# Performance work log

Measured on AMD Instinct MI355X. Metric: run time of the kernel, lower is better.

Reference implementation:

```python
import jax, jax.numpy as jnp
import numpy as np

B, F, V, D, K = 16384, 39, 30000, 16, 20
EPS = 1e-5


def bn_eval(x, g, b):
    # inference-mode BatchNorm1d with running_mean=0, running_var=1
    return g * x / jnp.sqrt(1.0 + EPS) + b


def setup_inputs() -> dict:
    key = jax.random.key(0)
    ks = jax.random.split(key, 12)
    x = jax.random.randint(ks[0], (B, F), 0, V)
    emb_table = jax.random.normal(ks[1], (F * V, D), dtype=jnp.float32) * 0.05
    w_c = jax.random.normal(ks[2], (F, F * D), dtype=jnp.float32) * 0.05
    w0 = jax.random.normal(ks[3], (1024, F * D), dtype=jnp.float32) * 0.04
    w1 = jax.random.normal(ks[4], (512, 1024), dtype=jnp.float32) * 0.03
    w_out = jax.random.normal(ks[5], (1, 512), dtype=jnp.float32) * 0.04
    return {
        'x': x, 'emb_table': emb_table,
        'w_c': w_c, 'b_c': jnp.zeros((F,)), 'g_c': jnp.ones((F,)), 'be_c': jnp.zeros((F,)),
        'w0': w0, 'b0': jnp.zeros((1024,)), 'g0': jnp.ones((1024,)), 'be0': jnp.zeros((1024,)),
        'w1': w1, 'b1': jnp.zeros((512,)), 'g1': jnp.ones((512,)), 'be1': jnp.zeros((512,)),
        'w_out': w_out, 'b_out': jnp.zeros((1,)),
    }


def reference(x, emb_table, w_c, b_c, g_c, be_c, w0, b0, g0, be0,
              w1, b1, g1, be1, w_out, b_out):
    offsets = jnp.arange(F, dtype=x.dtype) * V          # per-field offsets
    idx = x + offsets[None, :]                          # [B, F]
    emb = emb_table[idx]                                # [B, F, D] gather

    # controller_mlp: flatten (batch, D, F) layout like torch transpose(1,2)
    flat = jnp.transpose(emb, (0, 2, 1)).reshape(B, F * D)
    h = jax.nn.relu(bn_eval(flat @ w_c.T + b_c, g_c, be_c))
    scores = jax.nn.softmax(h, axis=1)                  # [B, F]

    # kmax_pooling: top-k field indices, sorted ascending, gather weights
    _, kidx = jax.lax.top_k(scores, K)
    kidx = jnp.sort(kidx, axis=1)                       # [B, K]
    w = jnp.take_along_axis(scores, kidx, axis=1)       # [B, K]

    # forward_select: gather selected field embeddings, weight them
    sel = jnp.take_along_axis(emb, kidx[:, :, None], axis=1)  # [B, K, D]
    weighted = sel * w[:, :, None]

    # scatter back into full field slots (unselected fields are zero)
    full = jnp.zeros((B, F, D), weighted.dtype)
    bidx = jnp.arange(B)[:, None]
    full = full.at[bidx, kidx].set(weighted)            # [B, F, D]

    z = jnp.transpose(full, (0, 2, 1)).reshape(B, F * D)
    z = jax.nn.relu(bn_eval(z @ w0.T + b0, g0, be0))
    z = jax.nn.relu(bn_eval(z @ w1.T + b1, g1, be1))
    out = jax.nn.sigmoid(z @ w_out.T + b_out)           # [B, 1]
    return out.squeeze(-1)
```

## Files before the change

### kernel.cpp

```cpp
#include <hip/hip_runtime.h>
#include <math.h>

#define B_SZ 16384
#define F_N 39
#define V_N 30000
#define D_N 16
#define K_SEL 20
#define FD 624
#define KP0 640
#define NCP 48
#define N0 1024
#define N1 512
#define CBR 16
#define ALD 648

typedef unsigned short u16;
typedef __attribute__((ext_vector_type(8))) short bf16x8;
typedef __attribute__((ext_vector_type(8))) unsigned short u16x8;
typedef __attribute__((ext_vector_type(4))) float f32x4;
typedef __attribute__((ext_vector_type(4))) unsigned short u16x4;

__device__ __forceinline__ u16 f2bf(float v) {
    union { float f; unsigned u; } x; x.f = v;
    unsigned r = x.u + 0x7fff + ((x.u >> 16) & 1);
    return (u16)(r >> 16);
}
__device__ __forceinline__ float bf2f(u16 v) {
    union { unsigned u; float f; } x; x.u = ((unsigned)v) << 16;
    return x.f;
}

#define GLD16(gp, lp) __builtin_amdgcn_global_load_lds( \
    (const __attribute__((address_space(1))) unsigned int*)(gp), \
    (__attribute__((address_space(3))) unsigned int*)(lp), 16, 0, 0)

#define PREP_W0 (N0 * KP0)
#define PREP_W1 (N1 * N0)
#define PREP_WC (NCP * KP0)
#define PREP_TOT (PREP_W0 + PREP_W1 + PREP_WC + 3 * NCP)

__global__ __launch_bounds__(256) void prep_all_kernel(
    const float* __restrict__ w0, const float* __restrict__ w1,
    const float* __restrict__ w_c, const float* __restrict__ b_c,
    const float* __restrict__ g_c, const float* __restrict__ be_c,
    u16* __restrict__ w0b, u16* __restrict__ w1b, u16* __restrict__ wcb,
    float* __restrict__ bcp, float* __restrict__ gcp, float* __restrict__ becp)
{
    int i = blockIdx.x * blockDim.x + threadIdx.x;
    if (i < PREP_W0) {
        int n = i / KP0, kk = i - n * KP0;
        float v = 0.f;
        if (kk < FD) v = w0[n * FD + (kk & 15) * F_N + (kk >> 4)];
        w0b[i] = f2bf(v);
        return;
    }
    i -= PREP_W0;
    if (i < PREP_W1) { w1b[i] = f2bf(w1[i]); return; }
    i -= PREP_W1;
    if (i < PREP_WC) {
        int n = i / KP0, kk = i - n * KP0;
        float v = 0.f;
        if (n < F_N && kk < FD) v = w_c[n * FD + (kk & 15) * F_N + (kk >> 4)];
        wcb[i] = f2bf(v);
        return;
    }
    i -= PREP_WC;
    if (i < 3 * NCP) {
        int which = i / NCP, n = i - which * NCP;
        float v = 0.f;
        if (n < F_N) v = (which == 0) ? b_c[n] : (which == 1) ? g_c[n] : be_c[n];
        ((which == 0) ? bcp : (which == 1) ? gcp : becp)[n] = v;
    }
}

__global__ __launch_bounds__(256) void fused_controller_kernel(
    const int* __restrict__ x, const float* __restrict__ emb_table,
    const u16* __restrict__ wcb, const float* __restrict__ bcp,
    const float* __restrict__ gcp, const float* __restrict__ becp,
    u16* __restrict__ zb)
{
    __shared__ __align__(16) u16 Al[CBR * ALD];
    __shared__ float vv[CBR][49];
    __shared__ f32x4 part[4][64][3];
    __shared__ float selw[CBR][F_N];

    const int t    = threadIdx.x;
    const int wave = t >> 6;
    const int lane = t & 63;
    const int b0   = blockIdx.x * CBR;

    for (int p = t; p < CBR * F_N; p += 256) {
        const int row = p / F_N;
        const int f   = p - row * F_N;
        const int xi  = x[b0 * F_N + p];
        const float4* src = (const float4*)(emb_table + (size_t)(xi + f * V_N) * D_N);
        float4 v0 = src[0], v1 = src[1], v2 = src[2], v3 = src[3];
        u16x8 o0 = { f2bf(v0.x), f2bf(v0.y), f2bf(v0.z), f2bf(v0.w),
                     f2bf(v1.x), f2bf(v1.y), f2bf(v1.z), f2bf(v1.w) };
        u16x8 o1 = { f2bf(v2.x), f2bf(v2.y), f2bf(v2.z), f2bf(v2.w),
                     f2bf(v3.x), f2bf(v3.y), f2bf(v3.z), f2bf(v3.w) };
        *(u16x8*)&Al[row * ALD + f * D_N]     = o0;
        *(u16x8*)&Al[row * ALD + f * D_N + 8] = o1;
    }
    __syncthreads();

    const int m = lane & 15;
    const int q = lane >> 4;
    f32x4 acc0 = {}, acc1 = {}, acc2 = {};
    {
        const u16* ap  = &Al[m * ALD + wave * 160 + q * 8];
        const u16* bp0 = wcb + (size_t)(0  + m) * KP0 + wave * 160 + q * 8;
        const u16* bp1 = wcb + (size_t)(16 + m) * KP0 + wave * 160 + q * 8;
        const u16* bp2 = wcb + (size_t)(32 + m) * KP0 + wave * 160 + q * 8;
        #pragma unroll
        for (int k = 0; k < 5; ++k) {
            bf16x8 af = *(const bf16x8*)ap;
            bf16x8 b0 = *(const bf16x8*)bp0;
            bf16x8 b1 = *(const bf16x8*)bp1;
            bf16x8 b2 = *(const bf16x8*)bp2;
            acc0 = __builtin_amdgcn_mfma_f32_16x16x32_bf16(af, b0, acc0, 0, 0, 0);
            acc1 = __builtin_amdgcn_mfma_f32_16x16x32_bf16(af, b1, acc1, 0, 0, 0);
            acc2 = __builtin_amdgcn_mfma_f32_16x16x32_bf16(af, b2, acc2, 0, 0, 0);
            ap += 32; bp0 += 32; bp1 += 32; bp2 += 32;
        }
    }
    part[wave][lane][0] = acc0;
    part[wave][lane][1] = acc1;
    part[wave][lane][2] = acc2;
    __syncthreads();

    {
        f32x4 r0 = part[0][lane][0] + part[1][lane][0] + part[2][lane][0] + part[3][lane][0];
        f32x4 r1 = part[0][lane][1] + part[1][lane][1] + part[2][lane][1] + part[3][lane][1];
        f32x4 r2 = part[0][lane][2] + part[1][lane][2] + part[2][lane][2] + part[3][lane][2];

        const float rs = rsqrtf(1.0f + 1e-5f);
        if (q == wave) {
            #pragma unroll
            for (int j = 0; j < 3; ++j) {
                const f32x4 a = (j == 0) ? r0 : (j == 1) ? r1 : r2;
                const int n = j * 16 + m;
                const float gn = gcp[n] * rs;
                const float bn = becp[n];
                const float bi = bcp[n];
                #pragma unroll
                for (int r = 0; r < 4; ++r)
                    vv[wave * 4 + r][n] = fmaxf(fmaf(gn, a[r] + bi, bn), 0.f);
            }
        }
    }
    __syncthreads();

    {
        const int row = wave * 4 + (lane >> 4);
        const int fl  = lane & 15;
        float e[3] = {0.f, 0.f, 0.f};
        float mloc = -1e30f;
        #pragma unroll
        for (int it = 0; it < 3; ++it) {
            const int f = fl + 16 * it;
            if (f < F_N) { e[it] = vv[row][f]; mloc = fmaxf(mloc, e[it]); }
        }
        mloc = fmaxf(mloc, __shfl_xor(mloc, 1, 64));
        mloc = fmaxf(mloc, __shfl_xor(mloc, 2, 64));
        mloc = fmaxf(mloc, __shfl_xor(mloc, 4, 64));
        mloc = fmaxf(mloc, __shfl_xor(mloc, 8, 64));
        float sloc = 0.f;
        #pragma unroll
        for (int it = 0; it < 3; ++it) {
            const int f = fl + 16 * it;
            if (f < F_N) { e[it] = expf(e[it] - mloc); sloc += e[it]; }
        }
        sloc += __shfl_xor(sloc, 1, 64);
        sloc += __shfl_xor(sloc, 2, 64);
        sloc += __shfl_xor(sloc, 4, 64);
        sloc += __shfl_xor(sloc, 8, 64);
        const float inv = 1.f / sloc;
        #pragma unroll
        for (int it = 0; it < 3; ++it) {
            const int f = fl + 16 * it;
            if (f < F_N) vv[row][f] = e[it];
        }

        int rank[3] = {};
        for (int gg = 0; gg < F_N; ++gg) {
            const float o = vv[row][gg];
            #pragma unroll
            for (int it = 0; it < 3; ++it) {
                const int f = fl + 16 * it;
                if (f < F_N)
                    rank[it] += (o > e[it] || (o == e[it] && gg < f)) ? 1 : 0;
            }
        }
        #pragma unroll
        for (int it = 0; it < 3; ++it) {
            const int f = fl + 16 * it;
            if (f < F_N)
                selw[row][f] = (rank[it] < K_SEL) ? e[it] * inv : 0.f;
        }
    }
    __syncthreads();

    for (int gp = t; gp < CBR * 40; gp += 256) {
        const int row  = gp & 15;
        const int slot = gp >> 4;
        u16* dst = zb + (size_t)(b0 + row) * KP0 + slot * D_N;
        u16x8 o0 = {0,0,0,0,0,0,0,0}, o1 = {0,0,0,0,0,0,0,0};
        if (slot < F_N) {
            const float w = selw[row][slot];
            u16x8 a0 = *(u16x8*)&Al[row * ALD + slot * D_N];
            u16x8 a1 = *(u16x8*)&Al[row * ALD + slot * D_N + 8];
            #pragma unroll
            for (int k = 0; k < 8; ++k) {
                o0[k] = f2bf(bf2f(a0[k]) * w);
                o1[k] = f2bf(bf2f(a1[k]) * w);
            }
        }
        *(u16x8*)dst = o0;
        *(u16x8*)(dst + 8) = o1;
    }
}

template<int MODE>
__global__ __launch_bounds__(256) void gemm_mfma_bn_relu(
    const u16* __restrict__ A, const u16* __restrict__ W,
    const float* __restrict__ bias, const float* __restrict__ g,
    const float* __restrict__ be, u16* __restrict__ Cout,
    int M, int N, int Kp,
    const float* __restrict__ w_out, float* __restrict__ outp)
{
    __shared__ __align__(16) u16 As[2][128 * 32];
    __shared__ __align__(16) u16 Bs[2][128 * 32];

    const int t    = threadIdx.x;
    const int wave = t >> 6;
    const int lane = t & 63;
    const int wm   = wave >> 1, wn = wave & 1;
    const int m0   = blockIdx.x * 128;
    const int n0   = blockIdx.y * 128;

    const int lr    = lane >> 2;
    const int swz_u = (lane & 3) ^ ((lane >> 3) & 3);
    const u16* gA0 = A + (size_t)(m0 + wave * 32 + lr) * Kp + swz_u * 8;
    const u16* gB0 = W + (size_t)(n0 + wave * 32 + lr) * Kp + swz_u * 8;
    const size_t kstep16 = 16 * (size_t)Kp;
    const int oA0 = (wave * 32) * 32;
    const int oA1 = (wave * 32 + 16) * 32;

    const int q    = lane >> 4;
    const int lr16 = lane & 15;

    int aoff[4], boff[4];
    #pragma unroll
    for (int i = 0; i < 4; ++i) {
        int ra = wm * 64 + i * 16 + lr16;
        aoff[i] = ra * 32 + ((q ^ ((ra >> 1) & 3)) * 8);
        int rb = wn * 64 + i * 16 + lr16;
        boff[i] = rb * 32 + ((q ^ ((rb >> 1) & 3)) * 8);
    }

    GLD16(gA0,           &As[0][oA0]);
    GLD16(gA0 + kstep16, &As[0][oA1]);
    GLD16(gB0,           &Bs[0][oA0]);
    GLD16(gB0 + kstep16, &Bs[0][oA1]);
    gA0 += 32; gB0 += 32;

    f32x4 acc[4][4] = {};
    int buf = 0;

    for (int k0 = 0; k0 < Kp; k0 += 32) {
        __syncthreads();
        if (k0 + 32 < Kp) {
            GLD16(gA0,           &As[buf ^ 1][oA0]);
            GLD16(gA0 + kstep16, &As[buf ^ 1][oA1]);
            GLD16(gB0,           &Bs[buf ^ 1][oA0]);
            GLD16(gB0 + kstep16, &Bs[buf ^ 1][oA1]);
            gA0 += 32; gB0 += 32;
        }

        bf16x8 af[4], bfr[4];
        #pragma unroll
        for (int i = 0; i < 4; ++i) af[i]  = *(const bf16x8*)&As[buf][aoff[i]];
        #pragma unroll
        for (int j = 0; j < 4; ++j) bfr[j] = *(const bf16x8*)&Bs[buf][boff[j]];

        #pragma unroll
        for (int i = 0; i < 4; ++i)
            #pragma unroll
            for (int j = 0; j < 4; ++j)
                acc[i][j] = __builtin_amdgcn_mfma_f32_16x16x32_bf16(
                    af[i], bfr[j], acc[i][j], 0, 0, 0);
        buf ^= 1;
    }

    const float rs = rsqrtf(1.0f + 1e-5f);
    if (MODE == 0) {
        #pragma unroll
        for (int j = 0; j < 4; ++j) {
            const int n = n0 + wn * 64 + j * 16 + lr16;
            const float bn_g = g[n] * rs;
            const float bn_b = be[n];
            const float bi   = bias[n];
            #pragma unroll
            for (int i = 0; i < 4; ++i) {
                const int mbase = m0 + wm * 64 + i * 16 + q * 4;
                #pragma unroll
                for (int r = 0; r < 4; ++r) {
                    float v = acc[i][j][r] + bi;
                    v = fmaxf(fmaf(bn_g, v, bn_b), 0.f);
                    Cout[(size_t)(mbase + r) * N + n] = f2bf(v);
                }
            }
        }
    } else {
        float s[4][4] = {};
        #pragma unroll
        for (int j = 0; j < 4; ++j) {
            const int n = n0 + wn * 64 + j * 16 + lr16;
            const float bn_g = g[n] * rs;
            const float bn_b = be[n];
            const float bi   = bias[n];
            const float wo   = w_out[n];
            #pragma unroll
            for (int i = 0; i < 4; ++i)
                #pragma unroll
                for (int r = 0; r < 4; ++r) {
                    float v = acc[i][j][r] + bi;
                    v = fmaxf(fmaf(bn_g, v, bn_b), 0.f);
                    s[i][r] = fmaf(v, wo, s[i][r]);
                }
        }
        #pragma unroll
        for (int i = 0; i < 4; ++i)
            #pragma unroll
            for (int r = 0; r < 4; ++r) {
                float v = s[i][r];
                v += __shfl_xor(v, 1, 64);
                v += __shfl_xor(v, 2, 64);
                v += __shfl_xor(v, 4, 64);
                v += __shfl_xor(v, 8, 64);
                s[i][r] = v;
            }
        if (lr16 == 0) {
            #pragma unroll
            for (int i = 0; i < 4; ++i) {
                const int mbase = m0 + wm * 64 + i * 16 + q * 4;
                #pragma unroll
                for (int r = 0; r < 4; ++r)
                    atomicAdd(&outp[mbase + r], s[i][r]);
            }
        }
    }
}

__global__ __launch_bounds__(256) void sigmoid_kernel(
    const float* __restrict__ outp, const float* __restrict__ b_out,
    float* __restrict__ out)
{
    const int b = blockIdx.x * 256 + threadIdx.x;
    out[b] = 1.f / (1.f + expf(-(outp[b] + b_out[0])));
}

extern "C" void kernel_launch(void* const* d_in, const int* in_sizes, int n_in,
                              void* d_out, int out_size, void* d_ws, size_t ws_size,
                              hipStream_t stream)
{
    const int*   x     = (const int*)  d_in[0];
    const float* emb   = (const float*)d_in[1];
    const float* w_c   = (const float*)d_in[2];
    const float* b_c   = (const float*)d_in[3];
    const float* g_c   = (const float*)d_in[4];
    const float* be_c  = (const float*)d_in[5];
    const float* w0    = (const float*)d_in[6];
    const float* b0    = (const float*)d_in[7];
    const float* g0    = (const float*)d_in[8];
    const float* be0   = (const float*)d_in[9];
    const float* w1    = (const float*)d_in[10];
    const float* b1    = (const float*)d_in[11];
    const float* g1    = (const float*)d_in[12];
    const float* be1   = (const float*)d_in[13];
    const float* w_out = (const float*)d_in[14];
    const float* b_out = (const float*)d_in[15];
    float* out = (float*)d_out;

    u16*   zb    = (u16*)d_ws;
    u16*   w0b   = zb    + (size_t)B_SZ * KP0;
    u16*   h0b   = w0b   + (size_t)N0 * KP0;
    u16*   w1b   = h0b   + (size_t)B_SZ * N0;
    u16*   wcb   = w1b   + (size_t)N1 * N0;
    float* outp  = (float*)(wcb + (size_t)NCP * KP0);
    float* bcp   = outp + B_SZ;
    float* gcp   = bcp + NCP;
    float* becp  = gcp + NCP;

    prep_all_kernel<<<(PREP_TOT + 255) / 256, 256, 0, stream>>>(
        w0, w1, w_c, b_c, g_c, be_c, w0b, w1b, wcb, bcp, gcp, becp);

    fused_controller_kernel<<<B_SZ / CBR, 256, 0, stream>>>(
        x, emb, wcb, bcp, gcp, becp, zb);

    gemm_mfma_bn_relu<0><<<dim3(B_SZ / 128, N0 / 128), 256, 0, stream>>>(
        zb, w0b, b0, g0, be0, h0b, B_SZ, N0, KP0, nullptr, nullptr);

    hipMemsetAsync(outp, 0, B_SZ * sizeof(float), stream);

    gemm_mfma_bn_relu<1><<<dim3(B_SZ / 128, N1 / 128), 256, 0, stream>>>(
        h0b, w1b, b1, g1, be1, nullptr, B_SZ, N1, N0, w_out, outp);

    sigmoid_kernel<<<B_SZ / 256, 256, 0, stream>>>(outp, b_out, out);
}
```

Measured before the change: 223.3 us.

## Enlarge GEMM0 tile to 256x128, fold outp zeroing into prep, unroll gather

The first MLP GEMM moves to its own kernel with 256x128 block tiles, where each wave computes 64x128 outputs through a 4x8 MFMA accumulator grid. This raises operand reuse per LDS load and halves the number of blocks along M. The hipMemsetAsync on the output accumulator is removed and the zeroing is done inside the prep kernel instead. The embedding gather loop is manually unrolled so all index loads are issued up front. The larger tile needs more registers and LDS, which may lower occupancy.

```diff
diff --git a/kernel.cpp b/kernel.cpp
--- a/kernel.cpp
+++ b/kernel.cpp
@@ -37,14 +37,15 @@
 #define PREP_W0 (N0 * KP0)
 #define PREP_W1 (N1 * N0)
 #define PREP_WC (NCP * KP0)
-#define PREP_TOT (PREP_W0 + PREP_W1 + PREP_WC + 3 * NCP)
+#define PREP_TOT (PREP_W0 + PREP_W1 + PREP_WC + 3 * NCP + B_SZ)
 
 __global__ __launch_bounds__(256) void prep_all_kernel(
     const float* __restrict__ w0, const float* __restrict__ w1,
     const float* __restrict__ w_c, const float* __restrict__ b_c,
     const float* __restrict__ g_c, const float* __restrict__ be_c,
     u16* __restrict__ w0b, u16* __restrict__ w1b, u16* __restrict__ wcb,
-    float* __restrict__ bcp, float* __restrict__ gcp, float* __restrict__ becp)
+    float* __restrict__ bcp, float* __restrict__ gcp, float* __restrict__ becp,
+    float* __restrict__ outp)
 {
     int i = blockIdx.x * blockDim.x + threadIdx.x;
     if (i < PREP_W0) {
@@ -70,7 +71,10 @@
         float v = 0.f;
         if (n < F_N) v = (which == 0) ? b_c[n] : (which == 1) ? g_c[n] : be_c[n];
         ((which == 0) ? bcp : (which == 1) ? gcp : becp)[n] = v;
-    }
+        return;
+    }
+    i -= 3 * NCP;
+    if (i < B_SZ) outp[i] = 0.f;
 }
 
 __global__ __launch_bounds__(256) void fused_controller_kernel(
@@ -89,18 +93,30 @@
     const int lane = t & 63;
     const int b0   = blockIdx.x * CBR;
 
-    for (int p = t; p < CBR * F_N; p += 256) {
-        const int row = p / F_N;
-        const int f   = p - row * F_N;
-        const int xi  = x[b0 * F_N + p];
-        const float4* src = (const float4*)(emb_table + (size_t)(xi + f * V_N) * D_N);
-        float4 v0 = src[0], v1 = src[1], v2 = src[2], v3 = src[3];
-        u16x8 o0 = { f2bf(v0.x), f2bf(v0.y), f2bf(v0.z), f2bf(v0.w),
-                     f2bf(v1.x), f2bf(v1.y), f2bf(v1.z), f2bf(v1.w) };
-        u16x8 o1 = { f2bf(v2.x), f2bf(v2.y), f2bf(v2.z), f2bf(v2.w),
-                     f2bf(v3.x), f2bf(v3.y), f2bf(v3.z), f2bf(v3.w) };
-        *(u16x8*)&Al[row * ALD + f * D_N]     = o0;
-        *(u16x8*)&Al[row * ALD + f * D_N + 8] = o1;
+    {
+        const int p0 = t, p1 = t + 256, p2 = t + 512;
+        const int xi0 = x[b0 * F_N + p0];
+        const int xi1 = x[b0 * F_N + p1];
+        const int xi2 = (p2 < CBR * F_N) ? x[b0 * F_N + p2] : 0;
+        const int pp[3] = { p0, p1, p2 };
+        const int xx[3] = { xi0, xi1, xi2 };
+        #pragma unroll
+        for (int s = 0; s < 3; ++s) {
+            const int p = pp[s];
+            if (p < CBR * F_N) {
+                const int row = p / F_N;
+                const int f   = p - row * F_N;
+                const float4* src =
+                    (const float4*)(emb_table + (size_t)(xx[s] + f * V_N) * D_N);
+                float4 v0 = src[0], v1 = src[1], v2 = src[2], v3 = src[3];
+                u16x8 o0 = { f2bf(v0.x), f2bf(v0.y), f2bf(v0.z), f2bf(v0.w),
+                             f2bf(v1.x), f2bf(v1.y), f2bf(v1.z), f2bf(v1.w) };
+                u16x8 o1 = { f2bf(v2.x), f2bf(v2.y), f2bf(v2.z), f2bf(v2.w),
+                             f2bf(v3.x), f2bf(v3.y), f2bf(v3.z), f2bf(v3.w) };
+                *(u16x8*)&Al[row * ALD + f * D_N]     = o0;
+                *(u16x8*)&Al[row * ALD + f * D_N + 8] = o1;
+            }
+        }
     }
     __syncthreads();
 
@@ -221,12 +237,103 @@
     }
 }
 
-template<int MODE>
-__global__ __launch_bounds__(256) void gemm_mfma_bn_relu(
+__global__ __launch_bounds__(256) void gemm0_256_kernel(
     const u16* __restrict__ A, const u16* __restrict__ W,
     const float* __restrict__ bias, const float* __restrict__ g,
     const float* __restrict__ be, u16* __restrict__ Cout,
-    int M, int N, int Kp,
+    int M, int N, int Kp)
+{
+    __shared__ __align__(16) u16 As[2][256 * 32];
+    __shared__ __align__(16) u16 Bs[2][128 * 32];
+
+    const int t    = threadIdx.x;
+    const int wave = t >> 6;
+    const int lane = t & 63;
+    const int m0   = blockIdx.x * 256;
+    const int n0   = blockIdx.y * 128;
+
+    const int lr    = lane >> 2;
+    const int swz_u = (lane & 3) ^ ((lane >> 3) & 3);
+    const u16* gA = A + (size_t)(m0 + wave * 64 + lr) * Kp + swz_u * 8;
+    const u16* gB = W + (size_t)(n0 + wave * 32 + lr) * Kp + swz_u * 8;
+    const size_t kst = 16 * (size_t)Kp;
+    const int oA = (wave * 64) * 32;
+    const int oB = (wave * 32) * 32;
+
+    const int q    = lane >> 4;
+    const int lr16 = lane & 15;
+
+    int aoff[4], boff[8];
+    #pragma unroll
+    for (int i = 0; i < 4; ++i) {
+        int ra = wave * 64 + i * 16 + lr16;
+        aoff[i] = ra * 32 + ((q ^ ((ra >> 1) & 3)) * 8);
+    }
+    #pragma unroll
+    for (int j = 0; j < 8; ++j) {
+        int rb = j * 16 + lr16;
+        boff[j] = rb * 32 + ((q ^ ((rb >> 1) & 3)) * 8);
+    }
+
+    #pragma unroll
+    for (int kk = 0; kk < 4; ++kk) GLD16(gA + kk * kst, &As[0][oA + kk * 16 * 32]);
+    #pragma unroll
+    for (int kk = 0; kk < 2; ++kk) GLD16(gB + kk * kst, &Bs[0][oB + kk * 16 * 32]);
+    gA += 32; gB += 32;
+
+    f32x4 acc[4][8] = {};
+
+    for (int k0 = 0; k0 < Kp; k0 += 32) {
+        const int buf = (k0 >> 5) & 1;
+        __syncthreads();
+        if (k0 + 32 < Kp) {
+            #pragma unroll
+            for (int kk = 0; kk < 4; ++kk)
+                GLD16(gA + kk * kst, &As[buf ^ 1][oA + kk * 16 * 32]);
+            #pragma unroll
+            for (int kk = 0; kk < 2; ++kk)
+                GLD16(gB + kk * kst, &Bs[buf ^ 1][oB + kk * 16 * 32]);
+            gA += 32; gB += 32;
+        }
+
+        bf16x8 af[4], bfr[8];
+        #pragma unroll
+        for (int i = 0; i < 4; ++i) af[i]  = *(const bf16x8*)&As[buf][aoff[i]];
+        #pragma unroll
+        for (int j = 0; j < 8; ++j) bfr[j] = *(const bf16x8*)&Bs[buf][boff[j]];
+
+        #pragma unroll
+        for (int i = 0; i < 4; ++i)
+            #pragma unroll
+            for (int j = 0; j < 8; ++j)
+                acc[i][j] = __builtin_amdgcn_mfma_f32_16x16x32_bf16(
+                    af[i], bfr[j], acc[i][j], 0, 0, 0);
+    }
+
+    const float rs = rsqrtf(1.0f + 1e-5f);
+    #pragma unroll
+    for (int j = 0; j < 8; ++j) {
+        const int n = n0 + j * 16 + lr16;
+        const float bn_g = g[n] * rs;
+        const float bn_b = be[n];
+        const float bi   = bias[n];
+        #pragma unroll
+        for (int i = 0; i < 4; ++i) {
+            const int mbase = m0 + wave * 64 + i * 16 + q * 4;
+            #pragma unroll
+            for (int r = 0; r < 4; ++r) {
+                float v = acc[i][j][r] + bi;
+                v = fmaxf(fmaf(bn_g, v, bn_b), 0.f);
+                Cout[(size_t)(mbase + r) * N + n] = f2bf(v);
+            }
+        }
+    }
+}
+
+__global__ __launch_bounds__(256) void gemm1_fused_out_kernel(
+    const u16* __restrict__ A, const u16* __restrict__ W,
+    const float* __restrict__ bias, const float* __restrict__ g,
+    const float* __restrict__ be, int M, int N, int Kp,
     const float* __restrict__ w_out, float* __restrict__ outp)
 {
     __shared__ __align__(16) u16 As[2][128 * 32];
@@ -266,9 +373,9 @@
     gA0 += 32; gB0 += 32;
 
     f32x4 acc[4][4] = {};
-    int buf = 0;
 
     for (int k0 = 0; k0 < Kp; k0 += 32) {
+        const int buf = (k0 >> 5) & 1;
         __syncthreads();
         if (k0 + 32 < Kp) {
             GLD16(gA0,           &As[buf ^ 1][oA0]);
@@ -290,65 +397,44 @@
             for (int j = 0; j < 4; ++j)
                 acc[i][j] = __builtin_amdgcn_mfma_f32_16x16x32_bf16(
                     af[i], bfr[j], acc[i][j], 0, 0, 0);
-        buf ^= 1;
     }
 
     const float rs = rsqrtf(1.0f + 1e-5f);
-    if (MODE == 0) {
-        #pragma unroll
-        for (int j = 0; j < 4; ++j) {
-            const int n = n0 + wn * 64 + j * 16 + lr16;
-            const float bn_g = g[n] * rs;
-            const float bn_b = be[n];
-            const float bi   = bias[n];
-            #pragma unroll
-            for (int i = 0; i < 4; ++i) {
-                const int mbase = m0 + wm * 64 + i * 16 + q * 4;
-                #pragma unroll
-                for (int r = 0; r < 4; ++r) {
-                    float v = acc[i][j][r] + bi;
-                    v = fmaxf(fmaf(bn_g, v, bn_b), 0.f);
-                    Cout[(size_t)(mbase + r) * N + n] = f2bf(v);
-                }
-            }
-        }
-    } else {
-        float s[4][4] = {};
-        #pragma unroll
-        for (int j = 0; j < 4; ++j) {
-            const int n = n0 + wn * 64 + j * 16 + lr16;
-            const float bn_g = g[n] * rs;
-            const float bn_b = be[n];
-            const float bi   = bias[n];
-            const float wo   = w_out[n];
-            #pragma unroll
-            for (int i = 0; i < 4; ++i)
-                #pragma unroll
-                for (int r = 0; r < 4; ++r) {
-                    float v = acc[i][j][r] + bi;
-                    v = fmaxf(fmaf(bn_g, v, bn_b), 0.f);
-                    s[i][r] = fmaf(v, wo, s[i][r]);
-                }
-        }
+    float s[4][4] = {};
+    #pragma unroll
+    for (int j = 0; j < 4; ++j) {
+        const int n = n0 + wn * 64 + j * 16 + lr16;
+        const float bn_g = g[n] * rs;
+        const float bn_b = be[n];
+        const float bi   = bias[n];
+        const float wo   = w_out[n];
         #pragma unroll
         for (int i = 0; i < 4; ++i)
             #pragma unroll
             for (int r = 0; r < 4; ++r) {
-                float v = s[i][r];
-                v += __shfl_xor(v, 1, 64);
-                v += __shfl_xor(v, 2, 64);
-                v += __shfl_xor(v, 4, 64);
-                v += __shfl_xor(v, 8, 64);
-                s[i][r] = v;
-            }
-        if (lr16 == 0) {
-            #pragma unroll
-            for (int i = 0; i < 4; ++i) {
-                const int mbase = m0 + wm * 64 + i * 16 + q * 4;
-                #pragma unroll
-                for (int r = 0; r < 4; ++r)
-                    atomicAdd(&outp[mbase + r], s[i][r]);
-            }
+                float v = acc[i][j][r] + bi;
+                v = fmaxf(fmaf(bn_g, v, bn_b), 0.f);
+                s[i][r] = fmaf(v, wo, s[i][r]);
+            }
+    }
+    #pragma unroll
+    for (int i = 0; i < 4; ++i)
+        #pragma unroll
+        for (int r = 0; r < 4; ++r) {
+            float v = s[i][r];
+            v += __shfl_xor(v, 1, 64);
+            v += __shfl_xor(v, 2, 64);
+            v += __shfl_xor(v, 4, 64);
+            v += __shfl_xor(v, 8, 64);
+            s[i][r] = v;
+        }
+    if (lr16 == 0) {
+        #pragma unroll
+        for (int i = 0; i < 4; ++i) {
+            const int mbase = m0 + wm * 64 + i * 16 + q * 4;
+            #pragma unroll
+            for (int r = 0; r < 4; ++r)
+                atomicAdd(&outp[mbase + r], s[i][r]);
         }
     }
 }
@@ -394,18 +480,16 @@
     float* becp  = gcp + NCP;
 
     prep_all_kernel<<<(PREP_TOT + 255) / 256, 256, 0, stream>>>(
-        w0, w1, w_c, b_c, g_c, be_c, w0b, w1b, wcb, bcp, gcp, becp);
+        w0, w1, w_c, b_c, g_c, be_c, w0b, w1b, wcb, bcp, gcp, becp, outp);
 
     fused_controller_kernel<<<B_SZ / CBR, 256, 0, stream>>>(
         x, emb, wcb, bcp, gcp, becp, zb);
 
-    gemm_mfma_bn_relu<0><<<dim3(B_SZ / 128, N0 / 128), 256, 0, stream>>>(
-        zb, w0b, b0, g0, be0, h0b, B_SZ, N0, KP0, nullptr, nullptr);
-
-    hipMemsetAsync(outp, 0, B_SZ * sizeof(float), stream);
-
-    gemm_mfma_bn_relu<1><<<dim3(B_SZ / 128, N1 / 128), 256, 0, stream>>>(
-        h0b, w1b, b1, g1, be1, nullptr, B_SZ, N1, N0, w_out, outp);
+    gemm0_256_kernel<<<dim3(B_SZ / 256, N0 / 128), 256, 0, stream>>>(
+        zb, w0b, b0, g0, be0, h0b, B_SZ, N0, KP0);
+
+    gemm1_fused_out_kernel<<<dim3(B_SZ / 128, N1 / 128), 256, 0, stream>>>(
+        h0b, w1b, b1, g1, be1, B_SZ, N1, N0, w_out, outp);
 
     sigmoid_kernel<<<B_SZ / 256, 256, 0, stream>>>(outp, b_out, out);
 }
```

New measurement: 228.5 us. 1.02x slower.

## Triple-buffer GEMM LDS loads, batch gather index loads, fold memset into prep

Applied to the files above, without the earlier changes.

The GEMM main loop moves from double to triple buffering, so the global-to-LDS prefetch runs two K-steps ahead and has more time to hide load latency. The cost is more LDS per block, which may lower occupancy. The controller kernel now loads all three embedding indices up front so the dependent gathers can be in flight together. The output memset is folded into the prep kernel, which removes one launch on the stream.

```diff
diff --git a/kernel.cpp b/kernel.cpp
--- a/kernel.cpp
+++ b/kernel.cpp
@@ -37,14 +37,15 @@
 #define PREP_W0 (N0 * KP0)
 #define PREP_W1 (N1 * N0)
 #define PREP_WC (NCP * KP0)
-#define PREP_TOT (PREP_W0 + PREP_W1 + PREP_WC + 3 * NCP)
+#define PREP_TOT (PREP_W0 + PREP_W1 + PREP_WC + 3 * NCP + B_SZ)
 
 __global__ __launch_bounds__(256) void prep_all_kernel(
     const float* __restrict__ w0, const float* __restrict__ w1,
     const float* __restrict__ w_c, const float* __restrict__ b_c,
     const float* __restrict__ g_c, const float* __restrict__ be_c,
     u16* __restrict__ w0b, u16* __restrict__ w1b, u16* __restrict__ wcb,
-    float* __restrict__ bcp, float* __restrict__ gcp, float* __restrict__ becp)
+    float* __restrict__ bcp, float* __restrict__ gcp, float* __restrict__ becp,
+    float* __restrict__ outp)
 {
     int i = blockIdx.x * blockDim.x + threadIdx.x;
     if (i < PREP_W0) {
@@ -70,7 +71,10 @@
         float v = 0.f;
         if (n < F_N) v = (which == 0) ? b_c[n] : (which == 1) ? g_c[n] : be_c[n];
         ((which == 0) ? bcp : (which == 1) ? gcp : becp)[n] = v;
-    }
+        return;
+    }
+    i -= 3 * NCP;
+    if (i < B_SZ) outp[i] = 0.f;
 }
 
 __global__ __launch_bounds__(256) void fused_controller_kernel(
@@ -89,18 +93,30 @@
     const int lane = t & 63;
     const int b0   = blockIdx.x * CBR;
 
-    for (int p = t; p < CBR * F_N; p += 256) {
-        const int row = p / F_N;
-        const int f   = p - row * F_N;
-        const int xi  = x[b0 * F_N + p];
-        const float4* src = (const float4*)(emb_table + (size_t)(xi + f * V_N) * D_N);
-        float4 v0 = src[0], v1 = src[1], v2 = src[2], v3 = src[3];
-        u16x8 o0 = { f2bf(v0.x), f2bf(v0.y), f2bf(v0.z), f2bf(v0.w),
-                     f2bf(v1.x), f2bf(v1.y), f2bf(v1.z), f2bf(v1.w) };
-        u16x8 o1 = { f2bf(v2.x), f2bf(v2.y), f2bf(v2.z), f2bf(v2.w),
-                     f2bf(v3.x), f2bf(v3.y), f2bf(v3.z), f2bf(v3.w) };
-        *(u16x8*)&Al[row * ALD + f * D_N]     = o0;
-        *(u16x8*)&Al[row * ALD + f * D_N + 8] = o1;
+    {
+        const int p0 = t, p1 = t + 256, p2 = t + 512;
+        const int xi0 = x[b0 * F_N + p0];
+        const int xi1 = x[b0 * F_N + p1];
+        const int xi2 = (p2 < CBR * F_N) ? x[b0 * F_N + p2] : 0;
+        const int pp[3] = { p0, p1, p2 };
+        const int xx[3] = { xi0, xi1, xi2 };
+        #pragma unroll
+        for (int s = 0; s < 3; ++s) {
+            const int p = pp[s];
+            if (p < CBR * F_N) {
+                const int row = p / F_N;
+                const int f   = p - row * F_N;
+                const float4* src =
+                    (const float4*)(emb_table + (size_t)(xx[s] + f * V_N) * D_N);
+                float4 v0 = src[0], v1 = src[1], v2 = src[2], v3 = src[3];
+                u16x8 o0 = { f2bf(v0.x), f2bf(v0.y), f2bf(v0.z), f2bf(v0.w),
+                             f2bf(v1.x), f2bf(v1.y), f2bf(v1.z), f2bf(v1.w) };
+                u16x8 o1 = { f2bf(v2.x), f2bf(v2.y), f2bf(v2.z), f2bf(v2.w),
+                             f2bf(v3.x), f2bf(v3.y), f2bf(v3.z), f2bf(v3.w) };
+                *(u16x8*)&Al[row * ALD + f * D_N]     = o0;
+                *(u16x8*)&Al[row * ALD + f * D_N + 8] = o1;
+            }
+        }
     }
     __syncthreads();
 
@@ -229,8 +245,8 @@
     int M, int N, int Kp,
     const float* __restrict__ w_out, float* __restrict__ outp)
 {
-    __shared__ __align__(16) u16 As[2][128 * 32];
-    __shared__ __align__(16) u16 Bs[2][128 * 32];
+    __shared__ __align__(16) u16 As[3][128 * 32];
+    __shared__ __align__(16) u16 Bs[3][128 * 32];
 
     const int t    = threadIdx.x;
     const int wave = t >> 6;
@@ -264,25 +280,30 @@
     GLD16(gB0,           &Bs[0][oA0]);
     GLD16(gB0 + kstep16, &Bs[0][oA1]);
     gA0 += 32; gB0 += 32;
+    GLD16(gA0,           &As[1][oA0]);
+    GLD16(gA0 + kstep16, &As[1][oA1]);
+    GLD16(gB0,           &Bs[1][oA0]);
+    GLD16(gB0 + kstep16, &Bs[1][oA1]);
+    gA0 += 32; gB0 += 32;
 
     f32x4 acc[4][4] = {};
-    int buf = 0;
+    int cur = 0, stg = 2;
 
     for (int k0 = 0; k0 < Kp; k0 += 32) {
         __syncthreads();
-        if (k0 + 32 < Kp) {
-            GLD16(gA0,           &As[buf ^ 1][oA0]);
-            GLD16(gA0 + kstep16, &As[buf ^ 1][oA1]);
-            GLD16(gB0,           &Bs[buf ^ 1][oA0]);
-            GLD16(gB0 + kstep16, &Bs[buf ^ 1][oA1]);
+        if (k0 + 64 < Kp) {
+            GLD16(gA0,           &As[stg][oA0]);
+            GLD16(gA0 + kstep16, &As[stg][oA1]);
+            GLD16(gB0,           &Bs[stg][oA0]);
+            GLD16(gB0 + kstep16, &Bs[stg][oA1]);
             gA0 += 32; gB0 += 32;
         }
 
         bf16x8 af[4], bfr[4];
         #pragma unroll
-        for (int i = 0; i < 4; ++i) af[i]  = *(const bf16x8*)&As[buf][aoff[i]];
-        #pragma unroll
-        for (int j = 0; j < 4; ++j) bfr[j] = *(const bf16x8*)&Bs[buf][boff[j]];
+        for (int i = 0; i < 4; ++i) af[i]  = *(const bf16x8*)&As[cur][aoff[i]];
+        #pragma unroll
+        for (int j = 0; j < 4; ++j) bfr[j] = *(const bf16x8*)&Bs[cur][boff[j]];
 
         #pragma unroll
         for (int i = 0; i < 4; ++i)
@@ -290,7 +311,9 @@
             for (int j = 0; j < 4; ++j)
                 acc[i][j] = __builtin_amdgcn_mfma_f32_16x16x32_bf16(
                     af[i], bfr[j], acc[i][j], 0, 0, 0);
-        buf ^= 1;
+
+        cur = (cur == 2) ? 0 : cur + 1;
+        stg = (stg == 2) ? 0 : stg + 1;
     }
 
     const float rs = rsqrtf(1.0f + 1e-5f);
@@ -394,7 +417,7 @@
     float* becp  = gcp + NCP;
 
     prep_all_kernel<<<(PREP_TOT + 255) / 256, 256, 0, stream>>>(
-        w0, w1, w_c, b_c, g_c, be_c, w0b, w1b, wcb, bcp, gcp, becp);
+        w0, w1, w_c, b_c, g_c, be_c, w0b, w1b, wcb, bcp, gcp, becp, outp);
 
     fused_controller_kernel<<<B_SZ / CBR, 256, 0, stream>>>(
         x, emb, wcb, bcp, gcp, becp, zb);
@@ -402,8 +425,6 @@
     gemm_mfma_bn_relu<0><<<dim3(B_SZ / 128, N0 / 128), 256, 0, stream>>>(
         zb, w0b, b0, g0, be0, h0b, B_SZ, N0, KP0, nullptr, nullptr);
 
-    hipMemsetAsync(outp, 0, B_SZ * sizeof(float), stream);
-
     gemm_mfma_bn_relu<1><<<dim3(B_SZ / 128, N1 / 128), 256, 0, stream>>>(
         h0b, w1b, b1, g1, be1, nullptr, B_SZ, N1, N0, w_out, outp);
 
```

After: 220.7 us. About the same (-1.2%).
